# Optimization experiments

Hardware: AMD Instinct MI355X
Metric: run time of the kernel (lower is better)

## Reference

```python
import jax, jax.numpy as jnp
import numpy as np

# LIF constants from norse.LIFParameters in the module
DT = 1e-3
TAU_MEM_INV = 4.0      # 1 / tau_mem, tau_mem = 0.25
TAU_SYN_INV = 200.0    # norse default 1/5e-3
V_TH = 0.1
ALPHA = 50.0           # super-spike surrogate slope
NHEAD = 4

@jax.custom_vjp
def spike(x):
    # SuperSpike: heaviside forward, surrogate gradient backward
    return (x > 0).astype(x.dtype)

def _spike_fwd(x):
    return spike(x), x

def _spike_bwd(x, g):
    return (g / (ALPHA * jnp.abs(x) + 1.0) ** 2,)

spike.defvjp(_spike_fwd, _spike_bwd)

def lif_reservoir(x, Win, Wres):
    # x: [B,S,I] -> spikes z: [B,S,R]. All batches start from zero state,
    # so the per-batch python loop of the original vectorizes over B.
    inp = jnp.einsum('bsi,ir->bsr', x, Win)  # precompute input currents
    B, S, R = inp.shape

    def step(carry, cur):  # cur: [B,R]
        v, i, z = carry
        total = cur + z @ Wres  # z=0 at t=0, matching the t>0 branch
        v_dec = v + DT * TAU_MEM_INV * (-v + i)  # v_leak = 0
        i_dec = i * (1.0 - DT * TAU_SYN_INV)
        z_new = spike(v_dec - V_TH)
        v_new = (1.0 - z_new) * v_dec            # v_reset = 0
        i_new = i_dec + total
        return (v_new, i_new, z_new), z_new

    init = (jnp.zeros((B, R), x.dtype),) * 3
    _, zs = jax.lax.scan(step, init, jnp.swapaxes(inp, 0, 1))
    return jnp.swapaxes(zs, 0, 1)  # [B,S,R]

def layer_norm(x, g, b, eps=1e-5):
    m = x.mean(-1, keepdims=True)
    v = ((x - m) ** 2).mean(-1, keepdims=True)
    return (x - m) / jnp.sqrt(v + eps) * g + b

def encoder_layer(x, Wqkv, bqkv, Wo, bo, g1, b1, g2, b2, W1, c1, W2, c2):
    # Post-norm TransformerEncoderLayer, relu activation, dropout=eval(0)
    B, S, D = x.shape
    dh = D // NHEAD
    qkv = x @ Wqkv.T + bqkv
    q, k, v = jnp.split(qkv, 3, axis=-1)
    rh = lambda t: t.reshape(B, S, NHEAD, dh)
    q, k, v = rh(q), rh(k), rh(v)
    scores = jnp.einsum('bqhd,bkhd->bhqk', q, k) / jnp.sqrt(jnp.asarray(dh, x.dtype))
    attn = jax.nn.softmax(scores, axis=-1)
    o = jnp.einsum('bhqk,bkhd->bqhd', attn, v).reshape(B, S, D)
    o = o @ Wo.T + bo
    x = layer_norm(x + o, g1, b1)
    ff = jax.nn.relu(x @ W1.T + c1) @ W2.T + c2
    return layer_norm(x + ff, g2, b2)

def setup_inputs() -> dict:
    key = jax.random.key(0)
    B, S, I, R, D, L, FF = 32, 1024, 8, 512, 256, 2, 1024
    ks = jax.random.split(key, 16)
    x = jax.random.normal(ks[0], (B, S, I), jnp.float32)
    Win = jax.random.normal(ks[1], (I, R), jnp.float32) * 0.1
    # sparse reservoir: density 0.2, values uniform [0,1)
    mask = (jax.random.uniform(ks[2], (R, R)) < 0.2).astype(jnp.float32)
    Wres = jax.random.uniform(ks[3], (R, R), jnp.float32) * mask
    Wread = jax.random.normal(ks[4], (D, R), jnp.float32) * 0.04
    bread = jnp.zeros((D,), jnp.float32)
    Wqkv = jax.random.normal(ks[5], (L, 3 * D, D), jnp.float32) * 0.05
    bqkv = jnp.zeros((L, 3 * D), jnp.float32)
    Wo = jax.random.normal(ks[6], (L, D, D), jnp.float32) * 0.05
    bo = jnp.zeros((L, D), jnp.float32)
    ln1_g = jnp.ones((L, D), jnp.float32)
    ln1_b = jnp.zeros((L, D), jnp.float32)
    ln2_g = jnp.ones((L, D), jnp.float32)
    ln2_b = jnp.zeros((L, D), jnp.float32)
    Wff1 = jax.random.normal(ks[7], (L, FF, D), jnp.float32) * 0.05
    bff1 = jnp.zeros((L, FF), jnp.float32)
    Wff2 = jax.random.normal(ks[8], (L, D, FF), jnp.float32) * 0.05
    bff2 = jnp.zeros((L, D), jnp.float32)
    return dict(x=x, Win=Win, Wres=Wres, Wread=Wread, bread=bread,
                Wqkv=Wqkv, bqkv=bqkv, Wo=Wo, bo=bo,
                ln1_g=ln1_g, ln1_b=ln1_b, ln2_g=ln2_g, ln2_b=ln2_b,
                Wff1=Wff1, bff1=bff1, Wff2=Wff2, bff2=bff2)

def reference(x, Win, Wres, Wread, bread, Wqkv, bqkv, Wo, bo,
              ln1_g, ln1_b, ln2_g, ln2_b, Wff1, bff1, Wff2, bff2):
    z = lif_reservoir(x, Win, Wres)          # [B,S,R] spike trains
    h = z @ Wread.T + bread                  # readout to transformer_dim
    for l in range(Wqkv.shape[0]):           # fixed small num_layers
        h = encoder_layer(h, Wqkv[l], bqkv[l], Wo[l], bo[l],
                          ln1_g[l], ln1_b[l], ln2_g[l], ln2_b[l],
                          Wff1[l], bff1[l], Wff2[l], bff2[l])
    return h
```

## Files before the change

kernel.cpp:

```cpp
#include <hip/hip_runtime.h>
#include <stdint.h>

using short8  = __attribute__((ext_vector_type(8))) short;
using floatx4 = __attribute__((ext_vector_type(4))) float;

typedef unsigned short u16;
typedef unsigned int u32;
typedef unsigned long long u64;

#define AS1(p) ((const __attribute__((address_space(1))) void*)(p))
#define AS3(p) ((__attribute__((address_space(3))) void*)(p))

__device__ __forceinline__ float bs2f(u16 u) { return __uint_as_float(((u32)u) << 16); }
__device__ __forceinline__ u16 f2bs(float f) {
  u32 x = __float_as_uint(f);
  x += 0x7FFFu + ((x >> 16) & 1u);
  return (u16)(x >> 16);
}
__device__ __forceinline__ float lo16(u32 u) { return __uint_as_float(u << 16); }
__device__ __forceinline__ float hi16(u32 u) { return __uint_as_float(u & 0xFFFF0000u); }

__global__ __launch_bounds__(256) void cvt_k(const float* __restrict__ src,
                                             u16* __restrict__ dst, int n) {
  int i = blockIdx.x * 256 + threadIdx.x;
  if (i < n) dst[i] = f2bs(src[i]);
}

__global__ __launch_bounds__(512) void inp_k(const float* __restrict__ x,
                                             const float* __restrict__ Win,
                                             float* __restrict__ inp) {
  const int row = blockIdx.x;
  const int r = threadIdx.x;
  const float* xr = x + (size_t)row * 8;
  float s = 0.f;
#pragma unroll
  for (int k = 0; k < 8; ++k) s = fmaf(Win[k * 512 + r], xr[k], s);
  inp[(size_t)row * 512 + r] = s;
}

__global__ __launch_bounds__(64) void reservoir_k(
    const float* __restrict__ inp,
    const float* __restrict__ Wres,
    u16* __restrict__ zout)
{
  const int b = blockIdx.x;
  const int c = threadIdx.x & 63;
  const float* ib = inp + (size_t)b * 524288 + c * 8;
  u16* zb = zout + (size_t)b * 524288 + c * 8;
  float v[8] = {}, ci[8] = {}, rec[8] = {};
  u32 pz = 0;
  float4 pa[8], pc[8];
#pragma unroll
  for (int u = 0; u < 8; ++u) {
    pa[u] = *(const float4*)(ib + (size_t)u * 512);
    pc[u] = *(const float4*)(ib + (size_t)u * 512 + 4);
  }
  for (int tb = 0; tb < 128; ++tb) {
    float4 na[8], nc[8];
    if (tb < 127) {
      const float* nb = ib + (size_t)(tb + 1) * 4096;
#pragma unroll
      for (int u = 0; u < 8; ++u) {
        na[u] = *(const float4*)(nb + (size_t)u * 512);
        nc[u] = *(const float4*)(nb + (size_t)u * 512 + 4);
      }
    }
#pragma unroll
    for (int u = 0; u < 8; ++u) {
      const int t = tb * 8 + u;
      const float in[8] = {pa[u].x, pa[u].y, pa[u].z, pa[u].w,
                           pc[u].x, pc[u].y, pc[u].z, pc[u].w};
      u32 nzb = 0;
      u32 zw[4];
#pragma unroll
      for (int j = 0; j < 8; ++j) {
        const float vdec = __fadd_rn(v[j], __fmul_rn(0.004f, __fadd_rn(-v[j], ci[j])));
        const int zc = (__fadd_rn(vdec, -0.1f) > 0.f) ? 1 : 0;
        v[j] = zc ? 0.f : vdec;
        nzb |= (u32)zc << j;
        ci[j] = __fadd_rn(__fmul_rn(ci[j], 0.8f), __fadd_rn(in[j], rec[j]));
        if (j & 1) zw[j >> 1] |= zc ? 0x3F800000u : 0u;
        else       zw[j >> 1]  = zc ? 0x3F80u : 0u;
      }
      *(uint4*)(zb + (size_t)t * 512) = make_uint4(zw[0], zw[1], zw[2], zw[3]);
      const u64 anyt = __ballot((nzb ^ pz) != 0);
      if (anyt) {
#pragma unroll
        for (int j = 0; j < 8; ++j) {
          const u64 nm = __ballot((nzb >> j) & 1);
          const u64 pm = __ballot((pz >> j) & 1);
          u64 on   = nm & ~pm;
          u64 offm = pm & ~nm;
          while (on) {
            const int cc = __builtin_ctzll(on); on &= on - 1;
            const float* wr = Wres + ((size_t)(cc * 8 + j) << 9) + c * 8;
            const float4 w0 = *(const float4*)wr;
            const float4 w1 = *(const float4*)(wr + 4);
            rec[0] += w0.x; rec[1] += w0.y; rec[2] += w0.z; rec[3] += w0.w;
            rec[4] += w1.x; rec[5] += w1.y; rec[6] += w1.z; rec[7] += w1.w;
          }
          while (offm) {
            const int cc = __builtin_ctzll(offm); offm &= offm - 1;
            const float* wr = Wres + ((size_t)(cc * 8 + j) << 9) + c * 8;
            const float4 w0 = *(const float4*)wr;
            const float4 w1 = *(const float4*)(wr + 4);
            rec[0] -= w0.x; rec[1] -= w0.y; rec[2] -= w0.z; rec[3] -= w0.w;
            rec[4] -= w1.x; rec[5] -= w1.y; rec[6] -= w1.z; rec[7] -= w1.w;
          }
        }
      }
      pz = nzb;
    }
    if (tb < 127) {
#pragma unroll
      for (int u = 0; u < 8; ++u) { pa[u] = na[u]; pc[u] = nc[u]; }
    }
  }
}

enum { MODE_BF16 = 0, MODE_F32 = 1, MODE_DUAL = 2, MODE_QKV = 3, MODE_AVC = 4 };

template <int WM, int WN, int MODE>
__global__ __launch_bounds__(WM * WN * 64) void gemm_bt(
    const u16* __restrict__ A, const u16* __restrict__ B,
    const float* __restrict__ bias, void* __restrict__ C0,
    void* __restrict__ C1, void* __restrict__ C2, int K, int lda, int ldb,
    int ldc, long long sA, long long sB, long long sC, int pair0, float scale,
    int relu)
{
  constexpr int BM = WM * 64, BN = WN * 64, BK = 32;
  constexpr int NT = WM * WN * 64;
  constexpr int CA = BM * 4 / NT, CB = BN * 4 / NT;
  __shared__ __align__(16) u16 As[BM * BK];
  __shared__ __align__(16) u16 Bs[BN * BK];
  const int tid = threadIdx.x;
  const int bz = blockIdx.z;
  const u16* Ab = A + (size_t)bz * sA + (size_t)blockIdx.y * BM * lda;
  const u16* Bb = B + (size_t)bz * sB + (size_t)blockIdx.x * BN * ldb;
  const int wavei = tid >> 6, lane = tid & 63;
  const int r16 = lane & 15, quad = lane >> 4;
  const int wm = (wavei % WM) * 64, wn = (wavei / WM) * 64;
  floatx4 acc[4][4] = {};
  for (int k0 = 0; k0 < K; k0 += BK) {
#pragma unroll
    for (int c = 0; c < CA; ++c) {
      const int idx = c * NT + tid;
      const int row = idx >> 2, kc = (idx & 3) << 3;
      __builtin_amdgcn_global_load_lds(AS1(Ab + (size_t)row * lda + k0 + kc),
                                       AS3(As + idx * 8), 16, 0, 0);
    }
#pragma unroll
    for (int c = 0; c < CB; ++c) {
      const int idx = c * NT + tid;
      const int row = idx >> 2, kc = (idx & 3) << 3;
      __builtin_amdgcn_global_load_lds(AS1(Bb + (size_t)row * ldb + k0 + kc),
                                       AS3(Bs + idx * 8), 16, 0, 0);
    }
    __syncthreads();
    short8 af[4], bfr[4];
#pragma unroll
    for (int i = 0; i < 4; ++i)
      af[i] = *(const short8*)&As[(wm + i * 16 + r16) * BK + quad * 8];
#pragma unroll
    for (int i = 0; i < 4; ++i)
      bfr[i] = *(const short8*)&Bs[(wn + i * 16 + r16) * BK + quad * 8];
#pragma unroll
    for (int i = 0; i < 4; ++i)
#pragma unroll
      for (int j = 0; j < 4; ++j)
        acc[i][j] = __builtin_amdgcn_mfma_f32_16x16x32_bf16(af[i], bfr[j], acc[i][j], 0, 0, 0);
    __syncthreads();
  }
#pragma unroll
  for (int i = 0; i < 4; ++i) {
#pragma unroll
    for (int j = 0; j < 4; ++j) {
#pragma unroll
      for (int q = 0; q < 4; ++q) {
        const int m = blockIdx.y * BM + wm + i * 16 + quad * 4 + q;
        const int n = blockIdx.x * BN + wn + j * 16 + r16;
        float val = acc[i][j][q] * scale;
        if (bias) val += bias[n];
        if (relu) val = fmaxf(val, 0.f);
        if constexpr (MODE == MODE_BF16) {
          ((u16*)C0)[(size_t)bz * sC + (size_t)m * ldc + n] = f2bs(val);
        } else if constexpr (MODE == MODE_F32) {
          ((float*)C0)[(size_t)m * ldc + n] = val;
        } else if constexpr (MODE == MODE_DUAL) {
          ((float*)C0)[(size_t)m * ldc + n] = val;
          ((u16*)C1)[(size_t)m * ldc + n] = f2bs(val);
        } else if constexpr (MODE == MODE_QKV) {
          const int b = m >> 10, s = m & 1023;
          const u16 outv = f2bs(val);
          const int h = (n & 255) >> 6, d = n & 63;
          if (n < 256)
            ((u16*)C0)[(((size_t)(b * 4 + h)) * 1024 + s) * 64 + d] = outv;
          else if (n < 512)
            ((u16*)C1)[(((size_t)(b * 4 + h)) * 1024 + s) * 64 + d] = outv;
          else
            ((u16*)C2)[(((size_t)(b * 4 + h)) * 64 + d) * 1024 + s] = outv;
        } else if constexpr (MODE == MODE_AVC) {
          const int p = pair0 + bz;
          const size_t coff = (size_t)(p >> 2) * 262144 + (size_t)(p & 3) * 64;
          ((u16*)C0)[coff + (size_t)m * 256 + n] = f2bs(val);
        }
      }
    }
  }
}

__global__ __launch_bounds__(256) void softmax_k(u16* __restrict__ s) {
  const int row = blockIdx.x * 4 + (threadIdx.x >> 6);
  const int lane = threadIdx.x & 63;
  u16* p = s + (size_t)row * 1024 + lane * 16;
  const uint4 u0 = *(const uint4*)p;
  const uint4 u1 = *(const uint4*)(p + 8);
  float f[16] = {lo16(u0.x), hi16(u0.x), lo16(u0.y), hi16(u0.y),
                 lo16(u0.z), hi16(u0.z), lo16(u0.w), hi16(u0.w),
                 lo16(u1.x), hi16(u1.x), lo16(u1.y), hi16(u1.y),
                 lo16(u1.z), hi16(u1.z), lo16(u1.w), hi16(u1.w)};
  float mx = f[0];
#pragma unroll
  for (int i = 1; i < 16; ++i) mx = fmaxf(mx, f[i]);
#pragma unroll
  for (int off = 32; off > 0; off >>= 1) mx = fmaxf(mx, __shfl_xor(mx, off));
  float sum = 0.f;
#pragma unroll
  for (int i = 0; i < 16; ++i) { f[i] = __expf(f[i] - mx); sum += f[i]; }
#pragma unroll
  for (int off = 32; off > 0; off >>= 1) sum += __shfl_xor(sum, off);
  const float inv = 1.f / sum;
  u32 o[8];
#pragma unroll
  for (int i = 0; i < 8; ++i)
    o[i] = (u32)f2bs(f[2 * i] * inv) | ((u32)f2bs(f[2 * i + 1] * inv) << 16);
  *(uint4*)p = make_uint4(o[0], o[1], o[2], o[3]);
  *(uint4*)(p + 8) = make_uint4(o[4], o[5], o[6], o[7]);
}

__global__ __launch_bounds__(256) void ln_k(const float* __restrict__ x,
                                            const float* __restrict__ add,
                                            const float* __restrict__ g,
                                            const float* __restrict__ bta,
                                            float* __restrict__ y32,
                                            u16* __restrict__ y16) {
  const int row = blockIdx.x * 4 + (threadIdx.x >> 6);
  const int lane = threadIdx.x & 63;
  const size_t base = (size_t)row * 256 + lane * 4;
  const float4 xv = *(const float4*)(x + base);
  const float4 av = *(const float4*)(add + base);
  float sv[4] = {xv.x + av.x, xv.y + av.y, xv.z + av.z, xv.w + av.w};
  float sum = sv[0] + sv[1] + sv[2] + sv[3];
#pragma unroll
  for (int off = 32; off > 0; off >>= 1) sum += __shfl_xor(sum, off);
  const float mean = sum * (1.f / 256.f);
  float var = 0.f;
  float d[4];
#pragma unroll
  for (int i = 0; i < 4; ++i) { d[i] = sv[i] - mean; var += d[i] * d[i]; }
#pragma unroll
  for (int off = 32; off > 0; off >>= 1) var += __shfl_xor(var, off);
  var *= (1.f / 256.f);
  const float inv = 1.f / sqrtf(var + 1e-5f);
  float yv[4];
#pragma unroll
  for (int i = 0; i < 4; ++i)
    yv[i] = d[i] * inv * g[lane * 4 + i] + bta[lane * 4 + i];
  if (y32) *(float4*)(y32 + base) = make_float4(yv[0], yv[1], yv[2], yv[3]);
  if (y16) {
    const u32 p0 = (u32)f2bs(yv[0]) | ((u32)f2bs(yv[1]) << 16);
    const u32 p1 = (u32)f2bs(yv[2]) | ((u32)f2bs(yv[3]) << 16);
    *(uint2*)(y16 + base) = make_uint2(p0, p1);
  }
}

extern "C" void kernel_launch(void* const* d_in, const int* in_sizes, int n_in,
                              void* d_out, int out_size, void* d_ws,
                              size_t ws_size, hipStream_t stream) {
  (void)in_sizes; (void)n_in; (void)out_size; (void)ws_size;
  const float* x     = (const float*)d_in[0];
  const float* Win   = (const float*)d_in[1];
  const float* Wres  = (const float*)d_in[2];
  const float* Wread = (const float*)d_in[3];
  const float* bread = (const float*)d_in[4];
  const float* Wqkv  = (const float*)d_in[5];
  const float* bqkv  = (const float*)d_in[6];
  const float* Wo    = (const float*)d_in[7];
  const float* bo    = (const float*)d_in[8];
  const float* g1    = (const float*)d_in[9];
  const float* b1    = (const float*)d_in[10];
  const float* g2    = (const float*)d_in[11];
  const float* b2    = (const float*)d_in[12];
  const float* W1    = (const float*)d_in[13];
  const float* c1    = (const float*)d_in[14];
  const float* W2    = (const float*)d_in[15];
  const float* c2    = (const float*)d_in[16];

  char* ws = (char*)d_ws;
  size_t off = 0;
  auto carve = [&](size_t bytes) {
    char* p = ws + off;
    off += (bytes + 255) & ~(size_t)255;
    return p;
  };
  u16* z      = (u16*)carve((size_t)32 * 1024 * 512 * 2);
  u16* wrd16  = (u16*)carve((size_t)256 * 512 * 2);
  u16* wqkv16 = (u16*)carve((size_t)2 * 768 * 256 * 2);
  u16* wo16   = (u16*)carve((size_t)2 * 256 * 256 * 2);
  u16* w116   = (u16*)carve((size_t)2 * 1024 * 256 * 2);
  u16* w216   = (u16*)carve((size_t)2 * 256 * 1024 * 2);
  u16* q_s    = (u16*)carve((size_t)128 * 1024 * 64 * 2);
  u16* k_s    = (u16*)carve((size_t)128 * 1024 * 64 * 2);
  u16* v_t    = (u16*)carve((size_t)128 * 64 * 1024 * 2);
  float* h32  = (float*)carve((size_t)32768 * 256 * 4);
  float* lin  = (float*)carve((size_t)32768 * 256 * 4);
  u16* h16    = (u16*)carve((size_t)32768 * 256 * 2);
  const int CH = 32;
  u16* ff1    = (u16*)carve((size_t)32768 * 1024 * 2);
  u16* o16    = h16;
  u16* scores = ff1;
  float* inp  = (float*)ff1;

  cvt_k<<<dim3(512), dim3(256), 0, stream>>>(Wread, wrd16, 131072);
  cvt_k<<<dim3(1536), dim3(256), 0, stream>>>(Wqkv, wqkv16, 393216);
  cvt_k<<<dim3(512), dim3(256), 0, stream>>>(Wo, wo16, 131072);
  cvt_k<<<dim3(2048), dim3(256), 0, stream>>>(W1, w116, 524288);
  cvt_k<<<dim3(2048), dim3(256), 0, stream>>>(W2, w216, 524288);

  inp_k<<<dim3(32768), dim3(512), 0, stream>>>(x, Win, inp);
  reservoir_k<<<dim3(32), dim3(64), 0, stream>>>(inp, Wres, z);

  gemm_bt<2, 2, MODE_DUAL><<<dim3(2, 256, 1), dim3(256), 0, stream>>>(
      z, wrd16, bread, h32, h16, nullptr, 512, 512, 512, 256, 0, 0, 0, 0, 1.0f, 0);

  for (int l = 0; l < 2; ++l) {
    gemm_bt<2, 2, MODE_QKV><<<dim3(6, 256, 1), dim3(256), 0, stream>>>(
        h16, wqkv16 + (size_t)l * 196608, bqkv + l * 768, q_s, k_s, v_t, 256,
        256, 256, 0, 0, 0, 0, 0, 1.0f, 0);
    for (int ch = 0; ch < 128; ch += CH) {
      gemm_bt<2, 2, MODE_BF16><<<dim3(8, 8, CH), dim3(256), 0, stream>>>(
          q_s + (size_t)ch * 65536, k_s + (size_t)ch * 65536, nullptr, scores,
          nullptr, nullptr, 64, 64, 64, 1024, 65536, 65536, 1048576, 0,
          0.125f, 0);
      softmax_k<<<dim3(256 * CH), dim3(256), 0, stream>>>(scores);
      gemm_bt<2, 1, MODE_AVC><<<dim3(1, 8, CH), dim3(128), 0, stream>>>(
          scores, v_t + (size_t)ch * 65536, nullptr, o16, nullptr, nullptr,
          1024, 1024, 1024, 0, 1048576, 65536, 0, ch, 1.0f, 0);
    }
    gemm_bt<2, 2, MODE_F32><<<dim3(2, 256, 1), dim3(256), 0, stream>>>(
        o16, wo16 + (size_t)l * 65536, bo + l * 256, lin, nullptr, nullptr,
        256, 256, 256, 256, 0, 0, 0, 0, 1.0f, 0);
    ln_k<<<dim3(8192), dim3(256), 0, stream>>>(h32, lin, g1 + l * 256,
                                               b1 + l * 256, h32, h16);
    gemm_bt<2, 2, MODE_BF16><<<dim3(8, 256, 1), dim3(256), 0, stream>>>(
        h16, w116 + (size_t)l * 262144, c1 + l * 1024, ff1, nullptr, nullptr,
        256, 256, 256, 1024, 0, 0, 0, 0, 1.0f, 1);
    gemm_bt<2, 2, MODE_F32><<<dim3(2, 256, 1), dim3(256), 0, stream>>>(
        ff1, w216 + (size_t)l * 262144, c2 + l * 256, lin, nullptr, nullptr,
        1024, 1024, 1024, 256, 0, 0, 0, 0, 1.0f, 0);
    float* y32 = (l == 1) ? (float*)d_out : h32;
    u16* y16 = (l == 1) ? nullptr : h16;
    ln_k<<<dim3(8192), dim3(256), 0, stream>>>(h32, lin, g2 + l * 256,
                                               b2 + l * 256, y32, y16);
  }
}
```

Baseline: 1.589 ms.

## Fuse QK^T, softmax and PV into a single flash-attention kernel

```diff
diff --git a/kernel.cpp b/kernel.cpp
--- a/kernel.cpp
+++ b/kernel.cpp
@@ -118,15 +118,14 @@
   }
 }
 
-enum { MODE_BF16 = 0, MODE_F32 = 1, MODE_DUAL = 2, MODE_QKV = 3, MODE_AVC = 4 };
+enum { MODE_BF16 = 0, MODE_F32 = 1, MODE_DUAL = 2, MODE_QKV = 3 };
 
 template <int WM, int WN, int MODE>
 __global__ __launch_bounds__(WM * WN * 64) void gemm_bt(
     const u16* __restrict__ A, const u16* __restrict__ B,
     const float* __restrict__ bias, void* __restrict__ C0,
     void* __restrict__ C1, void* __restrict__ C2, int K, int lda, int ldb,
-    int ldc, long long sA, long long sB, long long sC, int pair0, float scale,
-    int relu)
+    int ldc, long long sA, long long sB, long long sC, float scale, int relu)
 {
   constexpr int BM = WM * 64, BN = WN * 64, BK = 32;
   constexpr int NT = WM * WN * 64;
@@ -199,43 +198,165 @@
             ((u16*)C1)[(((size_t)(b * 4 + h)) * 1024 + s) * 64 + d] = outv;
           else
             ((u16*)C2)[(((size_t)(b * 4 + h)) * 64 + d) * 1024 + s] = outv;
-        } else if constexpr (MODE == MODE_AVC) {
-          const int p = pair0 + bz;
-          const size_t coff = (size_t)(p >> 2) * 262144 + (size_t)(p & 3) * 64;
-          ((u16*)C0)[coff + (size_t)m * 256 + n] = f2bs(val);
         }
       }
     }
   }
 }
 
-__global__ __launch_bounds__(256) void softmax_k(u16* __restrict__ s) {
-  const int row = blockIdx.x * 4 + (threadIdx.x >> 6);
-  const int lane = threadIdx.x & 63;
-  u16* p = s + (size_t)row * 1024 + lane * 16;
-  const uint4 u0 = *(const uint4*)p;
-  const uint4 u1 = *(const uint4*)(p + 8);
-  float f[16] = {lo16(u0.x), hi16(u0.x), lo16(u0.y), hi16(u0.y),
-                 lo16(u0.z), hi16(u0.z), lo16(u0.w), hi16(u0.w),
-                 lo16(u1.x), hi16(u1.x), lo16(u1.y), hi16(u1.y),
-                 lo16(u1.z), hi16(u1.z), lo16(u1.w), hi16(u1.w)};
-  float mx = f[0];
-#pragma unroll
-  for (int i = 1; i < 16; ++i) mx = fmaxf(mx, f[i]);
-#pragma unroll
-  for (int off = 32; off > 0; off >>= 1) mx = fmaxf(mx, __shfl_xor(mx, off));
-  float sum = 0.f;
-#pragma unroll
-  for (int i = 0; i < 16; ++i) { f[i] = __expf(f[i] - mx); sum += f[i]; }
-#pragma unroll
-  for (int off = 32; off > 0; off >>= 1) sum += __shfl_xor(sum, off);
-  const float inv = 1.f / sum;
-  u32 o[8];
-#pragma unroll
-  for (int i = 0; i < 8; ++i)
-    o[i] = (u32)f2bs(f[2 * i] * inv) | ((u32)f2bs(f[2 * i + 1] * inv) << 16);
-  *(uint4*)p = make_uint4(o[0], o[1], o[2], o[3]);
-  *(uint4*)(p + 8) = make_uint4(o[4], o[5], o[6], o[7]);
+__global__ __launch_bounds__(256) void attn_k(
+    const u16* __restrict__ q_s,
+    const u16* __restrict__ k_s,
+    const u16* __restrict__ v_t,
+    u16* __restrict__ o16)
+{
+  constexpr int LQ = 72, LV = 136, LP = 136;
+  __shared__ __align__(16) u16 Qs[128 * LQ];
+  __shared__ __align__(16) u16 Ks[128 * LQ];
+  __shared__ __align__(16) u16 Vt[64 * LV];
+  __shared__ __align__(16) u16 Ps[128 * LP];
+  const int tid = threadIdx.x;
+  const int w = tid >> 6, lane = tid & 63;
+  const int r16 = lane & 15, quad = lane >> 4;
+  const int p = blockIdx.y;
+  const int q0 = blockIdx.x * 128;
+  const u16* qg = q_s + ((size_t)p * 1024 + q0) * 64;
+  const u16* kg = k_s + (size_t)p * 65536;
+  const u16* vg = v_t + (size_t)p * 65536;
+
+#pragma unroll
+  for (int it = 0; it < 4; ++it) {
+    const int idx = it * 256 + tid;
+    const int row = idx >> 3, c8 = (idx & 7) * 8;
+    *(uint4*)&Qs[row * LQ + c8] = *(const uint4*)(qg + (size_t)row * 64 + c8);
+    *(uint4*)&Ks[row * LQ + c8] = *(const uint4*)(kg + (size_t)row * 64 + c8);
+  }
+#pragma unroll
+  for (int it = 0; it < 4; ++it) {
+    const int idx = it * 256 + tid;
+    const int row = idx >> 4, c8 = (idx & 15) * 8;
+    *(uint4*)&Vt[row * LV + c8] = *(const uint4*)(vg + (size_t)row * 1024 + c8);
+  }
+  __syncthreads();
+
+  short8 aq[2][2];
+#pragma unroll
+  for (int i = 0; i < 2; ++i)
+#pragma unroll
+    for (int kc = 0; kc < 2; ++kc)
+      aq[i][kc] = *(const short8*)&Qs[(w * 32 + i * 16 + r16) * LQ + kc * 32 + quad * 8];
+
+  floatx4 o[2][4] = {};
+  float mr[2][4], l[2][4];
+#pragma unroll
+  for (int i = 0; i < 2; ++i)
+#pragma unroll
+    for (int q = 0; q < 4; ++q) { mr[i][q] = -3e38f; l[i][q] = 0.f; }
+
+  for (int kt = 0; kt < 8; ++kt) {
+    uint4 kpre[4], vpre[4];
+    if (kt < 7) {
+      const u16* kgn = kg + (size_t)(kt + 1) * 128 * 64;
+#pragma unroll
+      for (int it = 0; it < 4; ++it) {
+        const int idx = it * 256 + tid;
+        kpre[it] = *(const uint4*)(kgn + (size_t)(idx >> 3) * 64 + (idx & 7) * 8);
+        vpre[it] = *(const uint4*)(vg + (size_t)(idx >> 4) * 1024 + (kt + 1) * 128 + (idx & 15) * 8);
+      }
+    }
+    floatx4 s[2][8] = {};
+#pragma unroll
+    for (int kc = 0; kc < 2; ++kc) {
+#pragma unroll
+      for (int f = 0; f < 8; ++f) {
+        const short8 bk = *(const short8*)&Ks[(f * 16 + r16) * LQ + kc * 32 + quad * 8];
+#pragma unroll
+        for (int i = 0; i < 2; ++i)
+          s[i][f] = __builtin_amdgcn_mfma_f32_16x16x32_bf16(aq[i][kc], bk, s[i][f], 0, 0, 0);
+      }
+    }
+#pragma unroll
+    for (int i = 0; i < 2; ++i) {
+      float mt[4] = {-3e38f, -3e38f, -3e38f, -3e38f};
+#pragma unroll
+      for (int f = 0; f < 8; ++f)
+#pragma unroll
+        for (int q = 0; q < 4; ++q) {
+          s[i][f][q] *= 0.125f;
+          mt[q] = fmaxf(mt[q], s[i][f][q]);
+        }
+#pragma unroll
+      for (int off = 8; off > 0; off >>= 1)
+#pragma unroll
+        for (int q = 0; q < 4; ++q) mt[q] = fmaxf(mt[q], __shfl_xor(mt[q], off));
+      float al[4], rs[4] = {};
+#pragma unroll
+      for (int q = 0; q < 4; ++q) {
+        const float mn = fmaxf(mr[i][q], mt[q]);
+        al[q] = __expf(mr[i][q] - mn);
+        mr[i][q] = mn;
+      }
+#pragma unroll
+      for (int f = 0; f < 8; ++f)
+#pragma unroll
+        for (int q = 0; q < 4; ++q) {
+          const float pv = __expf(s[i][f][q] - mr[i][q]);
+          s[i][f][q] = pv;
+          rs[q] += pv;
+        }
+#pragma unroll
+      for (int off = 8; off > 0; off >>= 1)
+#pragma unroll
+        for (int q = 0; q < 4; ++q) rs[q] += __shfl_xor(rs[q], off);
+#pragma unroll
+      for (int q = 0; q < 4; ++q) l[i][q] = l[i][q] * al[q] + rs[q];
+#pragma unroll
+      for (int n = 0; n < 4; ++n)
+#pragma unroll
+        for (int q = 0; q < 4; ++q) o[i][n][q] *= al[q];
+#pragma unroll
+      for (int f = 0; f < 8; ++f)
+#pragma unroll
+        for (int q = 0; q < 4; ++q)
+          Ps[(w * 32 + i * 16 + quad * 4 + q) * LP + f * 16 + r16] = f2bs(s[i][f][q]);
+    }
+#pragma unroll
+    for (int kc = 0; kc < 4; ++kc) {
+      short8 ap[2];
+#pragma unroll
+      for (int i = 0; i < 2; ++i)
+        ap[i] = *(const short8*)&Ps[(w * 32 + i * 16 + r16) * LP + kc * 32 + quad * 8];
+#pragma unroll
+      for (int n = 0; n < 4; ++n) {
+        const short8 bv = *(const short8*)&Vt[(n * 16 + r16) * LV + kc * 32 + quad * 8];
+#pragma unroll
+        for (int i = 0; i < 2; ++i)
+          o[i][n] = __builtin_amdgcn_mfma_f32_16x16x32_bf16(ap[i], bv, o[i][n], 0, 0, 0);
+      }
+    }
+    __syncthreads();
+    if (kt < 7) {
+#pragma unroll
+      for (int it = 0; it < 4; ++it) {
+        const int idx = it * 256 + tid;
+        *(uint4*)&Ks[(idx >> 3) * LQ + (idx & 7) * 8] = kpre[it];
+        *(uint4*)&Vt[(idx >> 4) * LV + (idx & 15) * 8] = vpre[it];
+      }
+      __syncthreads();
+    }
+  }
+  const int bb = p >> 2, hh = p & 3;
+#pragma unroll
+  for (int i = 0; i < 2; ++i)
+#pragma unroll
+    for (int q = 0; q < 4; ++q) {
+      const float inv = 1.f / l[i][q];
+      const int srow = q0 + w * 32 + i * 16 + quad * 4 + q;
+#pragma unroll
+      for (int n = 0; n < 4; ++n)
+        o16[((size_t)bb * 1024 + srow) * 256 + hh * 64 + n * 16 + r16] =
+            f2bs(o[i][n][q] * inv);
+    }
 }
 
 __global__ __launch_bounds__(256) void ln_k(const float* __restrict__ x,
@@ -315,10 +436,8 @@
   float* h32  = (float*)carve((size_t)32768 * 256 * 4);
   float* lin  = (float*)carve((size_t)32768 * 256 * 4);
   u16* h16    = (u16*)carve((size_t)32768 * 256 * 2);
-  const int CH = 32;
   u16* ff1    = (u16*)carve((size_t)32768 * 1024 * 2);
   u16* o16    = h16;
-  u16* scores = ff1;
   float* inp  = (float*)ff1;
 
   cvt_k<<<dim3(512), dim3(256), 0, stream>>>(Wread, wrd16, 131072);
@@ -331,33 +450,24 @@
   reservoir_k<<<dim3(32), dim3(64), 0, stream>>>(inp, Wres, z);
 
   gemm_bt<2, 2, MODE_DUAL><<<dim3(2, 256, 1), dim3(256), 0, stream>>>(
-      z, wrd16, bread, h32, h16, nullptr, 512, 512, 512, 256, 0, 0, 0, 0, 1.0f, 0);
+      z, wrd16, bread, h32, h16, nullptr, 512, 512, 512, 256, 0, 0, 0, 1.0f, 0);
 
   for (int l = 0; l < 2; ++l) {
     gemm_bt<2, 2, MODE_QKV><<<dim3(6, 256, 1), dim3(256), 0, stream>>>(
         h16, wqkv16 + (size_t)l * 196608, bqkv + l * 768, q_s, k_s, v_t, 256,
-        256, 256, 0, 0, 0, 0, 0, 1.0f, 0);
-    for (int ch = 0; ch < 128; ch += CH) {
-      gemm_bt<2, 2, MODE_BF16><<<dim3(8, 8, CH), dim3(256), 0, stream>>>(
-          q_s + (size_t)ch * 65536, k_s + (size_t)ch * 65536, nullptr, scores,
-          nullptr, nullptr, 64, 64, 64, 1024, 65536, 65536, 1048576, 0,
-          0.125f, 0);
-      softmax_k<<<dim3(256 * CH), dim3(256), 0, stream>>>(scores);
-      gemm_bt<2, 1, MODE_AVC><<<dim3(1, 8, CH), dim3(128), 0, stream>>>(
-          scores, v_t + (size_t)ch * 65536, nullptr, o16, nullptr, nullptr,
-          1024, 1024, 1024, 0, 1048576, 65536, 0, ch, 1.0f, 0);
-    }
+        256, 256, 0, 0, 0, 0, 1.0f, 0);
+    attn_k<<<dim3(8, 128), dim3(256), 0, stream>>>(q_s, k_s, v_t, o16);
     gemm_bt<2, 2, MODE_F32><<<dim3(2, 256, 1), dim3(256), 0, stream>>>(
         o16, wo16 + (size_t)l * 65536, bo + l * 256, lin, nullptr, nullptr,
-        256, 256, 256, 256, 0, 0, 0, 0, 1.0f, 0);
+        256, 256, 256, 256, 0, 0, 0, 1.0f, 0);
     ln_k<<<dim3(8192), dim3(256), 0, stream>>>(h32, lin, g1 + l * 256,
                                                b1 + l * 256, h32, h16);
     gemm_bt<2, 2, MODE_BF16><<<dim3(8, 256, 1), dim3(256), 0, stream>>>(
         h16, w116 + (size_t)l * 262144, c1 + l * 1024, ff1, nullptr, nullptr,
-        256, 256, 256, 1024, 0, 0, 0, 0, 1.0f, 1);
+        256, 256, 256, 1024, 0, 0, 0, 1.0f, 1);
     gemm_bt<2, 2, MODE_F32><<<dim3(2, 256, 1), dim3(256), 0, stream>>>(
         ff1, w216 + (size_t)l * 262144, c2 + l * 256, lin, nullptr, nullptr,
-        1024, 1024, 1024, 256, 0, 0, 0, 0, 1.0f, 0);
+        1024, 1024, 1024, 256, 0, 0, 0, 1.0f, 0);
     float* y32 = (l == 1) ? (float*)d_out : h32;
     u16* y16 = (l == 1) ? nullptr : h16;
     ln_k<<<dim3(8192), dim3(256), 0, stream>>>(h32, lin, g2 + l * 256,
```

Result: faster. 1.332 ms (-16.2%).
